# Kernel optimization log

Hardware: AMD Instinct MI355X
Metric: run time of the kernel (lower is better)

The kernel has to match this reference:

```python
import jax, jax.numpy as jnp
import numpy as np
import math

B, S, D, H = 16, 512, 1024, 16
DH = D // H  # 64
NUM_DEG = 50
NUM_SPE = 512


def setup_inputs() -> dict:
    key = jax.random.key(0)
    ks = jax.random.split(key, 16)
    w = lambda k, shape: (jax.random.normal(k, shape, jnp.float32) * 0.02)
    return {
        "hidden_states": jax.random.normal(ks[0], (B, S, D), jnp.float32),
        "attention_mask": jnp.zeros((B, 1, 1, S), jnp.float32),
        "if_2d": 1,
        "in_degree": jax.random.randint(ks[1], (B, S), 0, NUM_DEG),
        "out_degree": jax.random.randint(ks[2], (B, S), 0, NUM_DEG),
        "spe": jax.random.randint(ks[3], (B, S, S), 0, NUM_SPE),
        "dist_3d": jax.random.normal(ks[4], (B, S), jnp.float32),
        "dist_m": jax.random.normal(ks[5], (B, S, S), jnp.float32),
        # Linear params stored as [in, out]; y = x @ W + b
        "Wq": w(ks[6], (D, D)), "bq": jnp.zeros((D,), jnp.float32),
        "Wk": w(ks[7], (D, D)), "bk": jnp.zeros((D,), jnp.float32),
        "Wv": w(ks[8], (D, D)), "bv": jnp.zeros((D,), jnp.float32),
        "W_in": w(ks[9], (NUM_DEG, D)),
        "W_out": w(ks[10], (NUM_DEG, D)),
        "W_spe": w(ks[11], (NUM_SPE, H)),
    }


def reference(hidden_states, attention_mask, if_2d, in_degree, out_degree,
              spe, dist_3d, dist_m, Wq, bq, Wk, bk, Wv, bv,
              W_in, W_out, W_spe):
    # if_2d == True branch (2D graph path). padding_idx=0 -> row 0 is zero.
    pad_mask = (jnp.arange(NUM_DEG) != 0).astype(hidden_states.dtype)[:, None]
    pos = (W_in * pad_mask)[in_degree] + (W_out * pad_mask)[out_degree]  # [B,S,D]
    bias = jnp.transpose(W_spe[spe], (0, 3, 1, 2))  # [B,S,S,H] -> [B,H,S,S]

    h = hidden_states + pos
    to_heads = lambda x: x.reshape(B, S, H, DH).transpose(0, 2, 1, 3)  # [B,H,S,DH]
    q = to_heads(h @ Wq + bq)
    k = to_heads(h @ Wk + bk)
    v = to_heads(h @ Wv + bv)

    scores = jnp.einsum('bhqd,bhkd->bhqk', q, k) / math.sqrt(DH)
    scores = scores + bias + attention_mask
    probs = jax.nn.softmax(scores, axis=-1)  # dropout p=0 (eval)
    ctx = jnp.einsum('bhqk,bhkd->bhqd', probs, v)  # [B,H,S,DH]
    ctx = ctx.transpose(0, 2, 1, 3).reshape(B, S, D)
    return ctx, probs
```

## Files before the change

### kernel.cpp

```cpp
#include <hip/hip_runtime.h>

#define Bc 16
#define Sc 512
#define Dc 1024
#define Hc 16
#define DHc 64

#define AS1 __attribute__((address_space(1)))
#define AS3 __attribute__((address_space(3)))

typedef __attribute__((ext_vector_type(8))) __bf16 bf16x8;
typedef __attribute__((ext_vector_type(4))) float f32x4;
typedef __attribute__((ext_vector_type(8))) unsigned short ushort8;

static __device__ __forceinline__ unsigned short f2bf(float f) {
  unsigned int u = __builtin_bit_cast(unsigned int, f);
  unsigned int r = (u + 0x7fffu + ((u >> 16) & 1u)) >> 16;
  return (unsigned short)r;
}
static __device__ __forceinline__ float bf2f(unsigned short u) {
  unsigned int x = ((unsigned int)u) << 16;
  return __builtin_bit_cast(float, x);
}

__global__ __launch_bounds__(256) void k_prep(
    const float* __restrict__ hidden, const int* __restrict__ ind,
    const int* __restrict__ outd, const float* __restrict__ Win,
    const float* __restrict__ Wout, const float* __restrict__ Wq,
    const float* __restrict__ Wk, const float* __restrict__ Wv,
    const float* __restrict__ Wspe, unsigned short* __restrict__ hbf,
    unsigned short* __restrict__ Wtq, unsigned short* __restrict__ Wtk,
    unsigned short* __restrict__ Wtv, float* __restrict__ WspeT) {
  __shared__ float tile[64][65];
  int blk = blockIdx.x;
  int t = threadIdx.x;
  if (blk < 8192) {
    int row = blk;
    int id = ind[row], od = outd[row];
    float fi = (id != 0) ? 1.f : 0.f;
    float fo = (od != 0) ? 1.f : 0.f;
    float4 a = ((const float4*)(hidden + (size_t)row * Dc))[t];
    float4 x = ((const float4*)(Win + (size_t)id * Dc))[t];
    float4 y = ((const float4*)(Wout + (size_t)od * Dc))[t];
    ushort4 r;
    r.x = f2bf(a.x + fi * x.x + fo * y.x);
    r.y = f2bf(a.y + fi * x.y + fo * y.y);
    r.z = f2bf(a.z + fi * x.z + fo * y.z);
    r.w = f2bf(a.w + fi * x.w + fo * y.w);
    ((ushort4*)(hbf + (size_t)row * Dc))[t] = r;
  } else if (blk < 8960) {
    int f = blk - 8192;
    int z = f >> 8, rem = f & 255;
    int ky = rem >> 4, nx = rem & 15;
    const float* W = z == 0 ? Wq : z == 1 ? Wk : Wv;
    unsigned short* Wt = z == 0 ? Wtq : z == 1 ? Wtk : Wtv;
    int k0 = ky * 64, n0 = nx * 64;
    int r = t >> 4, c4 = (t & 15) * 4;
    for (int rr = r; rr < 64; rr += 16) {
      float4 v = *(const float4*)(W + (size_t)(k0 + rr) * Dc + n0 + c4);
      tile[rr][c4 + 0] = v.x;
      tile[rr][c4 + 1] = v.y;
      tile[rr][c4 + 2] = v.z;
      tile[rr][c4 + 3] = v.w;
    }
    __syncthreads();
    for (int rr = r; rr < 64; rr += 16) {
      ushort4 o;
      o.x = f2bf(tile[c4 + 0][rr]);
      o.y = f2bf(tile[c4 + 1][rr]);
      o.z = f2bf(tile[c4 + 2][rr]);
      o.w = f2bf(tile[c4 + 3][rr]);
      *(ushort4*)(Wt + (size_t)(n0 + rr) * Dc + k0 + c4) = o;
    }
  } else {
    int idx = (blk - 8960) * 256 + t;
    int h = idx >> 9, i = idx & 511;
    WspeT[idx] = Wspe[i * Hc + h];
  }
}

__global__ __launch_bounds__(256) void k_gemm_mfma(
    const unsigned short* __restrict__ hbf,
    const unsigned short* __restrict__ Wtq, const float* __restrict__ bq,
    const unsigned short* __restrict__ Wtk, const float* __restrict__ bk,
    const unsigned short* __restrict__ Wtv, const float* __restrict__ bv,
    unsigned short* __restrict__ Qo, unsigned short* __restrict__ Ko,
    unsigned short* __restrict__ Vt) {
  int zsel = blockIdx.z;
  const unsigned short* Wt;
  const float* bias;
  if (zsel == 0) { Wt = Wtq; bias = bq; }
  else if (zsel == 1) { Wt = Wtk; bias = bk; }
  else { Wt = Wtv; bias = bv; }

  __shared__ __align__(16) unsigned short As[128 * 32];
  __shared__ __align__(16) unsigned short Bs[128 * 32];

  int tid = threadIdx.x, lane = tid & 63, wave = tid >> 6;
  int m0 = blockIdx.y * 128, n0 = blockIdx.x * 128;
  int wr = wave >> 1, wc = wave & 1;

  f32x4 acc[4][4] = {};

  int srow = lane >> 2;
  int skb = (lane & 3) * 8;
  const unsigned short* gA = hbf + (size_t)(m0 + srow) * Dc + skb;
  const unsigned short* gB = Wt + (size_t)(n0 + srow) * Dc + skb;

  int fr = lane & 15, kg = (lane >> 4) * 8;

  for (int k0 = 0; k0 < Dc; k0 += 32) {
#pragma unroll
    for (int cc = 0; cc < 2; ++cc) {
      int c = wave + cc * 4;
      __builtin_amdgcn_global_load_lds(
          (const AS1 void*)(gA + (size_t)c * 16 * Dc + k0),
          (AS3 void*)(As + c * 16 * 32), 16, 0, 0);
      __builtin_amdgcn_global_load_lds(
          (const AS1 void*)(gB + (size_t)c * 16 * Dc + k0),
          (AS3 void*)(Bs + c * 16 * 32), 16, 0, 0);
    }
    __syncthreads();

    bf16x8 af[4], bfr[4];
#pragma unroll
    for (int m = 0; m < 4; ++m)
      af[m] = *(const bf16x8*)(As + (wr * 64 + m * 16 + fr) * 32 + kg);
#pragma unroll
    for (int n = 0; n < 4; ++n)
      bfr[n] = *(const bf16x8*)(Bs + (wc * 64 + n * 16 + fr) * 32 + kg);
#pragma unroll
    for (int m = 0; m < 4; ++m)
#pragma unroll
      for (int n = 0; n < 4; ++n)
        acc[m][n] = __builtin_amdgcn_mfma_f32_16x16x32_bf16(af[m], bfr[n], acc[m][n], 0, 0, 0);
    __syncthreads();
  }

  int fq = lane >> 4;
  if (zsel < 2) {
    unsigned short* C = (zsel == 0) ? Qo : Ko;
    float scale = (zsel == 0) ? 0.125f : 1.f;
#pragma unroll
    for (int m = 0; m < 4; ++m) {
#pragma unroll
      for (int n = 0; n < 4; ++n) {
        int col = n0 + wc * 64 + n * 16 + fr;
        float bb = bias[col];
#pragma unroll
        for (int r = 0; r < 4; ++r) {
          int row = m0 + wr * 64 + m * 16 + fq * 4 + r;
          C[(size_t)row * Dc + col] = f2bf((acc[m][n][r] + bb) * scale);
        }
      }
    }
  } else {
#pragma unroll
    for (int m = 0; m < 4; ++m) {
#pragma unroll
      for (int n = 0; n < 4; ++n) {
        int col = n0 + wc * 64 + n * 16 + fr;
        int hh = col >> 6, dh = col & 63;
        float bb = bias[col];
        int row = m0 + wr * 64 + m * 16 + fq * 4;
        int bb_ = row >> 9, ss = row & 511;
        ushort4 pk;
        pk.x = f2bf(acc[m][n][0] + bb);
        pk.y = f2bf(acc[m][n][1] + bb);
        pk.z = f2bf(acc[m][n][2] + bb);
        pk.w = f2bf(acc[m][n][3] + bb);
        *(ushort4*)(Vt + ((size_t)(bb_ * Hc + hh) * DHc + dh) * Sc + ss) = pk;
      }
    }
  }
}

#define SWB 520
__global__ __launch_bounds__(256, 8) void k_attn(
    const unsigned short* __restrict__ Qb, const unsigned short* __restrict__ Kb,
    const unsigned short* __restrict__ Vt, const int* __restrict__ spe,
    const float* __restrict__ WspeT, const float* __restrict__ mask,
    float* __restrict__ probs, float* __restrict__ ctx) {
  extern __shared__ char smem[];
  unsigned short* S = (unsigned short*)smem;
  float* Wb = (float*)(smem + 16640);
  float* Rinv = (float*)(smem + 16640 + 2048);

  int tid = threadIdx.x, lane = tid & 63, w = tid >> 6;
  int fr = lane & 15, fq = lane >> 4, kg8 = fq * 8;

  int flat = blockIdx.x;
  int swz = (flat & 7) * 1024 + (flat >> 3);
  int qt = swz & 31, h = (swz >> 5) & 15, b = swz >> 9;
  int q0 = qt * 16;

  for (int i = tid; i < 512; i += 256) Wb[i] = WspeT[h * 512 + i];

  const unsigned short* qbase = Qb + (size_t)(b * Sc + q0) * Dc + h * DHc;
  bf16x8 af[2];
#pragma unroll
  for (int kk = 0; kk < 2; ++kk)
    af[kk] = *(const bf16x8*)(qbase + (size_t)fr * Dc + kk * 32 + kg8);

  const unsigned short* kptr =
      Kb + (size_t)(b * Sc + w * 16 + fr) * Dc + h * DHc;
  bf16x8 kfA0 = *(const bf16x8*)(kptr + kg8);
  bf16x8 kfA1 = *(const bf16x8*)(kptr + 32 + kg8);
#pragma unroll
  for (int it = 0; it < 8; ++it) {
    bf16x8 kfB0, kfB1;
    if (it < 7) {
      const unsigned short* np = kptr + (size_t)(it + 1) * 64 * Dc;
      kfB0 = *(const bf16x8*)(np + kg8);
      kfB1 = *(const bf16x8*)(np + 32 + kg8);
    }
    f32x4 acc = {};
    __builtin_amdgcn_s_setprio(1);
    acc = __builtin_amdgcn_mfma_f32_16x16x32_bf16(kfA0, af[0], acc, 0, 0, 0);
    acc = __builtin_amdgcn_mfma_f32_16x16x32_bf16(kfA1, af[1], acc, 0, 0, 0);
    __builtin_amdgcn_s_setprio(0);
    ushort4 pk;
    pk.x = f2bf(acc[0]); pk.y = f2bf(acc[1]);
    pk.z = f2bf(acc[2]); pk.w = f2bf(acc[3]);
    *(ushort4*)(S + fr * SWB + it * 64 + w * 16 + fq * 4) = pk;
    kfA0 = kfB0; kfA1 = kfB1;
  }
  __syncthreads();

  {
    float* pbase = probs + (size_t)((b * Hc + h) * Sc + q0) * Sc;
    const int* spp0 = spe + (size_t)(b * Sc + q0 + w * 4) * Sc + lane * 8;
    float4 mk0 = *(const float4*)(mask + b * Sc + lane * 8);
    float4 mk1 = *(const float4*)(mask + b * Sc + lane * 8 + 4);
#pragma unroll
    for (int r4 = 0; r4 < 4; ++r4) {
      int row = w * 4 + r4;
      int4 i0 = *(const int4*)(spp0 + (size_t)r4 * Sc);
      int4 i1 = *(const int4*)(spp0 + (size_t)r4 * Sc + 4);
      ushort8 sv = *(const ushort8*)(S + row * SWB + lane * 8);
      float e0 = __expf(bf2f(sv[0]) + Wb[i0.x] + mk0.x);
      float e1 = __expf(bf2f(sv[1]) + Wb[i0.y] + mk0.y);
      float e2 = __expf(bf2f(sv[2]) + Wb[i0.z] + mk0.z);
      float e3 = __expf(bf2f(sv[3]) + Wb[i0.w] + mk0.w);
      float e4 = __expf(bf2f(sv[4]) + Wb[i1.x] + mk1.x);
      float e5 = __expf(bf2f(sv[5]) + Wb[i1.y] + mk1.y);
      float e6 = __expf(bf2f(sv[6]) + Wb[i1.z] + mk1.z);
      float e7 = __expf(bf2f(sv[7]) + Wb[i1.w] + mk1.w);
      ushort8 ev;
      ev[0] = f2bf(e0); ev[1] = f2bf(e1); ev[2] = f2bf(e2); ev[3] = f2bf(e3);
      ev[4] = f2bf(e4); ev[5] = f2bf(e5); ev[6] = f2bf(e6); ev[7] = f2bf(e7);
      *(ushort8*)(S + row * SWB + lane * 8) = ev;
      float sum = e0 + e1 + e2 + e3 + e4 + e5 + e6 + e7;
#pragma unroll
      for (int o = 32; o; o >>= 1) sum += __shfl_xor(sum, o);
      float rinv = 1.f / sum;
      f32x4 p0, p1;
      p0[0] = e0 * rinv; p0[1] = e1 * rinv; p0[2] = e2 * rinv; p0[3] = e3 * rinv;
      p1[0] = e4 * rinv; p1[1] = e5 * rinv; p1[2] = e6 * rinv; p1[3] = e7 * rinv;
      float* pdst = pbase + (size_t)row * Sc + lane * 8;
      __builtin_nontemporal_store(p0, (f32x4*)pdst);
      __builtin_nontemporal_store(p1, (f32x4*)(pdst + 4));
      if (lane == 0) Rinv[row] = rinv;
    }
  }
  asm volatile("s_waitcnt lgkmcnt(0)" ::: "memory");
  __builtin_amdgcn_s_barrier();
  __builtin_amdgcn_sched_barrier(0);

  const unsigned short* vptr =
      Vt + ((size_t)(b * Hc + h) * DHc + w * 16 + fr) * Sc;
  f32x4 pacc0 = {}, pacc1 = {};
  bf16x8 vfA0 = *(const bf16x8*)(vptr + kg8);
  bf16x8 vfA1 = *(const bf16x8*)(vptr + 32 + kg8);
#pragma unroll
  for (int it = 0; it < 8; ++it) {
    bf16x8 vfB0, vfB1;
    if (it < 7) {
      vfB0 = *(const bf16x8*)(vptr + (it + 1) * 64 + kg8);
      vfB1 = *(const bf16x8*)(vptr + (it + 1) * 64 + 32 + kg8);
    }
    bf16x8 pfr0 = *(const bf16x8*)(S + fr * SWB + it * 64 + kg8);
    bf16x8 pfr1 = *(const bf16x8*)(S + fr * SWB + it * 64 + 32 + kg8);
    __builtin_amdgcn_s_setprio(1);
    pacc0 = __builtin_amdgcn_mfma_f32_16x16x32_bf16(vfA0, pfr0, pacc0, 0, 0, 0);
    pacc1 = __builtin_amdgcn_mfma_f32_16x16x32_bf16(vfA1, pfr1, pacc1, 0, 0, 0);
    __builtin_amdgcn_s_setprio(0);
    vfA0 = vfB0; vfA1 = vfB1;
  }

  {
    float rv = Rinv[fr];
    f32x4 o;
    o[0] = (pacc0[0] + pacc1[0]) * rv;
    o[1] = (pacc0[1] + pacc1[1]) * rv;
    o[2] = (pacc0[2] + pacc1[2]) * rv;
    o[3] = (pacc0[3] + pacc1[3]) * rv;
    __builtin_nontemporal_store(
        o, (f32x4*)(ctx + (size_t)(b * Sc + q0 + fr) * Dc + h * DHc + w * 16 + fq * 4));
  }
}

extern "C" void kernel_launch(void* const* d_in, const int* in_sizes, int n_in,
                              void* d_out, int out_size, void* d_ws, size_t ws_size,
                              hipStream_t stream) {
  const float* hidden = (const float*)d_in[0];
  const float* amask = (const float*)d_in[1];
  const int* ind = (const int*)d_in[3];
  const int* outd = (const int*)d_in[4];
  const int* spe = (const int*)d_in[5];
  const float* Wq = (const float*)d_in[8];
  const float* bq = (const float*)d_in[9];
  const float* Wk = (const float*)d_in[10];
  const float* bk = (const float*)d_in[11];
  const float* Wv = (const float*)d_in[12];
  const float* bv = (const float*)d_in[13];
  const float* Win = (const float*)d_in[14];
  const float* Wout = (const float*)d_in[15];
  const float* Wspe = (const float*)d_in[16];

  char* ws = (char*)d_ws;
  const size_t BSD = (size_t)Bc * Sc * Dc;
  unsigned short* hbf = (unsigned short*)ws;
  unsigned short* Wtq = (unsigned short*)(ws + 16u * 1048576);
  unsigned short* Wtk = (unsigned short*)(ws + 18u * 1048576);
  unsigned short* Wtv = (unsigned short*)(ws + 20u * 1048576);
  float* WspeT = (float*)(ws + 22u * 1048576);
  unsigned short* Qb = (unsigned short*)(ws + 24u * 1048576);
  unsigned short* Kb = (unsigned short*)(ws + 40u * 1048576);
  unsigned short* Vt = (unsigned short*)(ws + 56u * 1048576);
  float* ctx = (float*)d_out;
  float* probs = (float*)d_out + BSD;

  (void)hipFuncSetAttribute((const void*)k_attn,
                            hipFuncAttributeMaxDynamicSharedMemorySize, 18752);

  k_prep<<<dim3(8992), 256, 0, stream>>>(hidden, ind, outd, Win, Wout, Wq, Wk,
                                         Wv, Wspe, hbf, Wtq, Wtk, Wtv, WspeT);
  k_gemm_mfma<<<dim3(8, 64, 3), 256, 0, stream>>>(hbf, Wtq, bq, Wtk, bk, Wtv, bv, Qb, Kb, Vt);
  k_attn<<<dim3(8192), 256, 18752, stream>>>(Qb, Kb, Vt, spe, WspeT, amask, probs, ctx);
}
```

Before: 247.7 us.

## Process four query tiles per attention block and interleave probs stores with PV MFMA

The attention kernel now has each block loop over four consecutive 16-row query tiles, with the grid reduced to a quarter of its former size. This amortizes the per-block W_spe bias-table load and the mask loads, and the block swizzle is reworked to fit. The normalized probs write is moved out of the softmax pass into the P·V loop, reading the bf16 exponentials back from LDS so global stores overlap the MFMA work. The LDS row stride is also padded from 520 to 528. The costs are extra barriers per tile, fewer blocks to hide latency, and probs computed from bf16-rounded exponentials, which is a small precision loss.

```diff
diff --git a/kernel.cpp b/kernel.cpp
--- a/kernel.cpp
+++ b/kernel.cpp
@@ -175,7 +175,7 @@
   }
 }
 
-#define SWB 520
+#define SWB 528
 __global__ __launch_bounds__(256, 8) void k_attn(
     const unsigned short* __restrict__ Qb, const unsigned short* __restrict__ Kb,
     const unsigned short* __restrict__ Vt, const int* __restrict__ spe,
@@ -183,120 +183,131 @@
     float* __restrict__ probs, float* __restrict__ ctx) {
   extern __shared__ char smem[];
   unsigned short* S = (unsigned short*)smem;
-  float* Wb = (float*)(smem + 16640);
-  float* Rinv = (float*)(smem + 16640 + 2048);
+  float* Wb = (float*)(smem + 16896);
+  float* Rinv = (float*)(smem + 16896 + 2048);
 
   int tid = threadIdx.x, lane = tid & 63, w = tid >> 6;
   int fr = lane & 15, fq = lane >> 4, kg8 = fq * 8;
 
-  int flat = blockIdx.x;
-  int swz = (flat & 7) * 1024 + (flat >> 3);
-  int qt = swz & 31, h = (swz >> 5) & 15, b = swz >> 9;
-  int q0 = qt * 16;
+  int blk = blockIdx.x;
+  int bh = (blk & 7) * 32 + ((blk >> 3) & 31);
+  int qtg = blk >> 8;
+  int h = bh & 15, b = bh >> 4;
 
   for (int i = tid; i < 512; i += 256) Wb[i] = WspeT[h * 512 + i];
-
-  const unsigned short* qbase = Qb + (size_t)(b * Sc + q0) * Dc + h * DHc;
-  bf16x8 af[2];
-#pragma unroll
-  for (int kk = 0; kk < 2; ++kk)
-    af[kk] = *(const bf16x8*)(qbase + (size_t)fr * Dc + kk * 32 + kg8);
-
   const unsigned short* kptr =
       Kb + (size_t)(b * Sc + w * 16 + fr) * Dc + h * DHc;
-  bf16x8 kfA0 = *(const bf16x8*)(kptr + kg8);
-  bf16x8 kfA1 = *(const bf16x8*)(kptr + 32 + kg8);
-#pragma unroll
-  for (int it = 0; it < 8; ++it) {
-    bf16x8 kfB0, kfB1;
-    if (it < 7) {
-      const unsigned short* np = kptr + (size_t)(it + 1) * 64 * Dc;
-      kfB0 = *(const bf16x8*)(np + kg8);
-      kfB1 = *(const bf16x8*)(np + 32 + kg8);
-    }
-    f32x4 acc = {};
-    __builtin_amdgcn_s_setprio(1);
-    acc = __builtin_amdgcn_mfma_f32_16x16x32_bf16(kfA0, af[0], acc, 0, 0, 0);
-    acc = __builtin_amdgcn_mfma_f32_16x16x32_bf16(kfA1, af[1], acc, 0, 0, 0);
-    __builtin_amdgcn_s_setprio(0);
-    ushort4 pk;
-    pk.x = f2bf(acc[0]); pk.y = f2bf(acc[1]);
-    pk.z = f2bf(acc[2]); pk.w = f2bf(acc[3]);
-    *(ushort4*)(S + fr * SWB + it * 64 + w * 16 + fq * 4) = pk;
-    kfA0 = kfB0; kfA1 = kfB1;
-  }
-  __syncthreads();
-
-  {
-    float* pbase = probs + (size_t)((b * Hc + h) * Sc + q0) * Sc;
-    const int* spp0 = spe + (size_t)(b * Sc + q0 + w * 4) * Sc + lane * 8;
-    float4 mk0 = *(const float4*)(mask + b * Sc + lane * 8);
-    float4 mk1 = *(const float4*)(mask + b * Sc + lane * 8 + 4);
-#pragma unroll
-    for (int r4 = 0; r4 < 4; ++r4) {
-      int row = w * 4 + r4;
-      int4 i0 = *(const int4*)(spp0 + (size_t)r4 * Sc);
-      int4 i1 = *(const int4*)(spp0 + (size_t)r4 * Sc + 4);
-      ushort8 sv = *(const ushort8*)(S + row * SWB + lane * 8);
-      float e0 = __expf(bf2f(sv[0]) + Wb[i0.x] + mk0.x);
-      float e1 = __expf(bf2f(sv[1]) + Wb[i0.y] + mk0.y);
-      float e2 = __expf(bf2f(sv[2]) + Wb[i0.z] + mk0.z);
-      float e3 = __expf(bf2f(sv[3]) + Wb[i0.w] + mk0.w);
-      float e4 = __expf(bf2f(sv[4]) + Wb[i1.x] + mk1.x);
-      float e5 = __expf(bf2f(sv[5]) + Wb[i1.y] + mk1.y);
-      float e6 = __expf(bf2f(sv[6]) + Wb[i1.z] + mk1.z);
-      float e7 = __expf(bf2f(sv[7]) + Wb[i1.w] + mk1.w);
-      ushort8 ev;
-      ev[0] = f2bf(e0); ev[1] = f2bf(e1); ev[2] = f2bf(e2); ev[3] = f2bf(e3);
-      ev[4] = f2bf(e4); ev[5] = f2bf(e5); ev[6] = f2bf(e6); ev[7] = f2bf(e7);
-      *(ushort8*)(S + row * SWB + lane * 8) = ev;
-      float sum = e0 + e1 + e2 + e3 + e4 + e5 + e6 + e7;
-#pragma unroll
-      for (int o = 32; o; o >>= 1) sum += __shfl_xor(sum, o);
-      float rinv = 1.f / sum;
-      f32x4 p0, p1;
-      p0[0] = e0 * rinv; p0[1] = e1 * rinv; p0[2] = e2 * rinv; p0[3] = e3 * rinv;
-      p1[0] = e4 * rinv; p1[1] = e5 * rinv; p1[2] = e6 * rinv; p1[3] = e7 * rinv;
-      float* pdst = pbase + (size_t)row * Sc + lane * 8;
-      __builtin_nontemporal_store(p0, (f32x4*)pdst);
-      __builtin_nontemporal_store(p1, (f32x4*)(pdst + 4));
-      if (lane == 0) Rinv[row] = rinv;
-    }
-  }
-  asm volatile("s_waitcnt lgkmcnt(0)" ::: "memory");
-  __builtin_amdgcn_s_barrier();
-  __builtin_amdgcn_sched_barrier(0);
-
   const unsigned short* vptr =
       Vt + ((size_t)(b * Hc + h) * DHc + w * 16 + fr) * Sc;
-  f32x4 pacc0 = {}, pacc1 = {};
-  bf16x8 vfA0 = *(const bf16x8*)(vptr + kg8);
-  bf16x8 vfA1 = *(const bf16x8*)(vptr + 32 + kg8);
-#pragma unroll
-  for (int it = 0; it < 8; ++it) {
-    bf16x8 vfB0, vfB1;
-    if (it < 7) {
-      vfB0 = *(const bf16x8*)(vptr + (it + 1) * 64 + kg8);
-      vfB1 = *(const bf16x8*)(vptr + (it + 1) * 64 + 32 + kg8);
-    }
-    bf16x8 pfr0 = *(const bf16x8*)(S + fr * SWB + it * 64 + kg8);
-    bf16x8 pfr1 = *(const bf16x8*)(S + fr * SWB + it * 64 + 32 + kg8);
-    __builtin_amdgcn_s_setprio(1);
-    pacc0 = __builtin_amdgcn_mfma_f32_16x16x32_bf16(vfA0, pfr0, pacc0, 0, 0, 0);
-    pacc1 = __builtin_amdgcn_mfma_f32_16x16x32_bf16(vfA1, pfr1, pacc1, 0, 0, 0);
-    __builtin_amdgcn_s_setprio(0);
-    vfA0 = vfB0; vfA1 = vfB1;
-  }
-
-  {
-    float rv = Rinv[fr];
-    f32x4 o;
-    o[0] = (pacc0[0] + pacc1[0]) * rv;
-    o[1] = (pacc0[1] + pacc1[1]) * rv;
-    o[2] = (pacc0[2] + pacc1[2]) * rv;
-    o[3] = (pacc0[3] + pacc1[3]) * rv;
-    __builtin_nontemporal_store(
-        o, (f32x4*)(ctx + (size_t)(b * Sc + q0 + fr) * Dc + h * DHc + w * 16 + fq * 4));
+  float4 mk0 = *(const float4*)(mask + b * Sc + lane * 8);
+  float4 mk1 = *(const float4*)(mask + b * Sc + lane * 8 + 4);
+
+  for (int item = 0; item < 4; ++item) {
+    int q0 = (qtg * 4 + item) * 16;
+    __syncthreads();
+
+    const unsigned short* qbase = Qb + (size_t)(b * Sc + q0) * Dc + h * DHc;
+    bf16x8 af0 = *(const bf16x8*)(qbase + (size_t)fr * Dc + kg8);
+    bf16x8 af1 = *(const bf16x8*)(qbase + (size_t)fr * Dc + 32 + kg8);
+
+    bf16x8 kfA0 = *(const bf16x8*)(kptr + kg8);
+    bf16x8 kfA1 = *(const bf16x8*)(kptr + 32 + kg8);
+#pragma unroll
+    for (int it = 0; it < 8; ++it) {
+      bf16x8 kfB0, kfB1;
+      if (it < 7) {
+        const unsigned short* np = kptr + (size_t)(it + 1) * 64 * Dc;
+        kfB0 = *(const bf16x8*)(np + kg8);
+        kfB1 = *(const bf16x8*)(np + 32 + kg8);
+      }
+      f32x4 acc = {};
+      __builtin_amdgcn_s_setprio(1);
+      acc = __builtin_amdgcn_mfma_f32_16x16x32_bf16(kfA0, af0, acc, 0, 0, 0);
+      acc = __builtin_amdgcn_mfma_f32_16x16x32_bf16(kfA1, af1, acc, 0, 0, 0);
+      __builtin_amdgcn_s_setprio(0);
+      ushort4 pk;
+      pk.x = f2bf(acc[0]); pk.y = f2bf(acc[1]);
+      pk.z = f2bf(acc[2]); pk.w = f2bf(acc[3]);
+      *(ushort4*)(S + fr * SWB + it * 64 + w * 16 + fq * 4) = pk;
+      kfA0 = kfB0; kfA1 = kfB1;
+    }
+    __syncthreads();
+
+    float ri0, ri1, ri2, ri3;
+    {
+      const int* spp0 = spe + (size_t)(b * Sc + q0 + w * 4) * Sc + lane * 8;
+#pragma unroll
+      for (int r4 = 0; r4 < 4; ++r4) {
+        int row = w * 4 + r4;
+        int4 i0 = *(const int4*)(spp0 + (size_t)r4 * Sc);
+        int4 i1 = *(const int4*)(spp0 + (size_t)r4 * Sc + 4);
+        ushort8 sv = *(const ushort8*)(S + row * SWB + lane * 8);
+        float e0 = __expf(bf2f(sv[0]) + Wb[i0.x] + mk0.x);
+        float e1 = __expf(bf2f(sv[1]) + Wb[i0.y] + mk0.y);
+        float e2 = __expf(bf2f(sv[2]) + Wb[i0.z] + mk0.z);
+        float e3 = __expf(bf2f(sv[3]) + Wb[i0.w] + mk0.w);
+        float e4 = __expf(bf2f(sv[4]) + Wb[i1.x] + mk1.x);
+        float e5 = __expf(bf2f(sv[5]) + Wb[i1.y] + mk1.y);
+        float e6 = __expf(bf2f(sv[6]) + Wb[i1.z] + mk1.z);
+        float e7 = __expf(bf2f(sv[7]) + Wb[i1.w] + mk1.w);
+        float sum = e0 + e1 + e2 + e3 + e4 + e5 + e6 + e7;
+#pragma unroll
+        for (int o = 32; o; o >>= 1) sum += __shfl_xor(sum, o);
+        float rinv = 1.f / sum;
+        if (r4 == 0) ri0 = rinv;
+        else if (r4 == 1) ri1 = rinv;
+        else if (r4 == 2) ri2 = rinv;
+        else ri3 = rinv;
+        ushort8 ev;
+        ev[0] = f2bf(e0); ev[1] = f2bf(e1); ev[2] = f2bf(e2); ev[3] = f2bf(e3);
+        ev[4] = f2bf(e4); ev[5] = f2bf(e5); ev[6] = f2bf(e6); ev[7] = f2bf(e7);
+        *(ushort8*)(S + row * SWB + lane * 8) = ev;
+        if (lane == 0) Rinv[row] = rinv;
+      }
+    }
+    __syncthreads();
+
+    float* pbase = probs + (size_t)((b * Hc + h) * Sc + q0) * Sc;
+    int prow = tid >> 4, pc0 = (tid & 15) * 4;
+    float prv = (fq == 0) ? ri0 : (fq == 1) ? ri1 : (fq == 2) ? ri2 : ri3;
+    f32x4 pacc0 = {}, pacc1 = {};
+    bf16x8 vfA0 = *(const bf16x8*)(vptr + kg8);
+    bf16x8 vfA1 = *(const bf16x8*)(vptr + 32 + kg8);
+    ushort4 svA = *(const ushort4*)(S + prow * SWB + pc0);
+#pragma unroll
+    for (int it = 0; it < 8; ++it) {
+      bf16x8 vfB0, vfB1;
+      ushort4 svB;
+      if (it < 7) {
+        vfB0 = *(const bf16x8*)(vptr + (it + 1) * 64 + kg8);
+        vfB1 = *(const bf16x8*)(vptr + (it + 1) * 64 + 32 + kg8);
+        svB = *(const ushort4*)(S + prow * SWB + (it + 1) * 64 + pc0);
+      }
+      {
+        f32x4 e;
+        e[0] = bf2f(svA.x) * prv; e[1] = bf2f(svA.y) * prv;
+        e[2] = bf2f(svA.z) * prv; e[3] = bf2f(svA.w) * prv;
+        __builtin_nontemporal_store(e, (f32x4*)(pbase + (size_t)prow * Sc + it * 64 + pc0));
+      }
+      bf16x8 pfr0 = *(const bf16x8*)(S + fr * SWB + it * 64 + kg8);
+      bf16x8 pfr1 = *(const bf16x8*)(S + fr * SWB + it * 64 + 32 + kg8);
+      __builtin_amdgcn_s_setprio(1);
+      pacc0 = __builtin_amdgcn_mfma_f32_16x16x32_bf16(vfA0, pfr0, pacc0, 0, 0, 0);
+      pacc1 = __builtin_amdgcn_mfma_f32_16x16x32_bf16(vfA1, pfr1, pacc1, 0, 0, 0);
+      __builtin_amdgcn_s_setprio(0);
+      vfA0 = vfB0; vfA1 = vfB1; svA = svB;
+    }
+
+    {
+      float rv = Rinv[fr];
+      f32x4 o;
+      o[0] = (pacc0[0] + pacc1[0]) * rv;
+      o[1] = (pacc0[1] + pacc1[1]) * rv;
+      o[2] = (pacc0[2] + pacc1[2]) * rv;
+      o[3] = (pacc0[3] + pacc1[3]) * rv;
+      __builtin_nontemporal_store(
+          o, (f32x4*)(ctx + (size_t)(b * Sc + q0 + fr) * Dc + h * DHc + w * 16 + fq * 4));
+    }
   }
 }
 
@@ -332,10 +343,10 @@
   float* probs = (float*)d_out + BSD;
 
   (void)hipFuncSetAttribute((const void*)k_attn,
-                            hipFuncAttributeMaxDynamicSharedMemorySize, 18752);
+                            hipFuncAttributeMaxDynamicSharedMemorySize, 19008);
 
   k_prep<<<dim3(8992), 256, 0, stream>>>(hidden, ind, outd, Win, Wout, Wq, Wk,
                                          Wv, Wspe, hbf, Wtq, Wtk, Wtv, WspeT);
   k_gemm_mfma<<<dim3(8, 64, 3), 256, 0, stream>>>(hbf, Wtq, bq, Wtk, bk, Wtv, bv, Qb, Kb, Vt);
-  k_attn<<<dim3(8192), 256, 18752, stream>>>(Qb, Kb, Vt, spe, WspeT, amask, probs, ctx);
-}
+  k_attn<<<dim3(2048), 256, 19008, stream>>>(Qb, Kb, Vt, spe, WspeT, amask, probs, ctx);
+}
```

After: 431.2 us. 74.1% more time.
